# Kernel tuning notes

Measured on AMD Instinct MI355X. Metric: run time of the kernel, lower is better.

## Reference

```python
import jax, jax.numpy as jnp
import numpy as np

D_MODEL = 768
H = 12
D_K = D_MODEL // H
B = 2
S = 2048
NEG = -1e9


def setup_inputs() -> dict:
    key = jax.random.key(0)
    ks = jax.random.split(key, 12)
    scale = 1.0 / np.sqrt(D_MODEL)
    inp = {
        "q": jax.random.normal(ks[0], (B, S, D_MODEL), jnp.float32),
        "k": jax.random.normal(ks[1], (B, S, D_MODEL), jnp.float32),
        "v": jax.random.normal(ks[2], (B, S, D_MODEL), jnp.float32),
        "mask": jax.random.randint(ks[3], (B, 1, S, S), 0, 2, jnp.int32),
        "Wq": jax.random.normal(ks[4], (D_MODEL, D_MODEL), jnp.float32) * scale,
        "bq": jnp.zeros((D_MODEL,), jnp.float32),
        "Wk": jax.random.normal(ks[5], (D_MODEL, D_MODEL), jnp.float32) * scale,
        "bk": jnp.zeros((D_MODEL,), jnp.float32),
        "Wv": jax.random.normal(ks[6], (D_MODEL, D_MODEL), jnp.float32) * scale,
        "bv": jnp.zeros((D_MODEL,), jnp.float32),
        "Wo": jax.random.normal(ks[7], (D_MODEL, D_MODEL), jnp.float32) * scale,
        "bo": jnp.zeros((D_MODEL,), jnp.float32),
    }
    return inp


def _split_heads(x):
    # [B, S, D] -> [B, H, S, D_K]
    b, s, _ = x.shape
    return x.reshape(b, s, H, D_K).transpose(0, 2, 1, 3)


def reference(q, k, v, mask, Wq, bq, Wk, bk, Wv, bv, Wo, bo):
    # torch Linear: x @ W.T + b
    query = _split_heads(q @ Wq.T + bq)
    key_ = _split_heads(k @ Wk.T + bk)
    value = _split_heads(v @ Wv.T + bv)

    scores = jnp.einsum("bhqd,bhkd->bhqk", query, key_) / np.sqrt(D_K)
    scores = jnp.where(mask == 0, NEG, scores)
    attn = jax.nn.softmax(scores, axis=-1)  # dropout p=0.0 -> identity

    x = jnp.einsum("bhqk,bhkd->bhqd", attn, value)
    x = x.transpose(0, 2, 1, 3).reshape(q.shape[0], -1, D_MODEL)
    return x @ Wo.T + bo
```

## Files before the change

### kernel.cpp

```cpp
#include <hip/hip_runtime.h>
#include <math.h>

#define DMODEL 768
#define NHEAD 12
#define DKDIM 64
#define BB 2
#define SS 2048
#define MROWS (BB * SS)
#define WELEM (DMODEL * DMODEL)

typedef unsigned short bf16_t;
typedef __attribute__((ext_vector_type(8))) short s8;
typedef __attribute__((ext_vector_type(4))) float f4;

#define MFMA(a, b, c) __builtin_amdgcn_mfma_f32_16x16x32_bf16((a), (b), (c), 0, 0, 0)

__device__ __forceinline__ bf16_t f2bf(float f) {
    unsigned u = __float_as_uint(f);
    u += 0x7fffu + ((u >> 16) & 1u);
    return (bf16_t)(u >> 16);
}
__device__ __forceinline__ unsigned pack2(float a, float b) {
    return (unsigned)f2bf(a) | ((unsigned)f2bf(b) << 16);
}
__device__ __forceinline__ s8 ldfrag(const bf16_t* p) {
    union { uint4 u; s8 s; } x;
    x.u = *(const uint4*)p;
    return x.s;
}

__device__ __forceinline__ void ld_stage(const bf16_t* p, uint4& u0, uint4& u1) {
    u0 = *(const uint4*)p;
    u1 = *(const uint4*)(p + 8);
}
__device__ __forceinline__ void ld_stage(const float* p, uint4& u0, uint4& u1) {
    const float4 f0 = *(const float4*)p;
    const float4 f1 = *(const float4*)(p + 4);
    const float4 f2 = *(const float4*)(p + 8);
    const float4 f3 = *(const float4*)(p + 12);
    u0.x = pack2(f0.x, f0.y); u0.y = pack2(f0.z, f0.w);
    u0.z = pack2(f1.x, f1.y); u0.w = pack2(f1.z, f1.w);
    u1.x = pack2(f2.x, f2.y); u1.y = pack2(f2.z, f2.w);
    u1.z = pack2(f3.x, f3.y); u1.w = pack2(f3.z, f3.w);
}

__global__ void cvt_weights(const float* __restrict__ W0, const float* __restrict__ W1,
                            const float* __restrict__ W2, const float* __restrict__ W3,
                            bf16_t* __restrict__ dst)
{
    const float* src = (blockIdx.y == 0) ? W0 : (blockIdx.y == 1) ? W1
                     : (blockIdx.y == 2) ? W2 : W3;
    bf16_t* d = dst + (size_t)blockIdx.y * WELEM;
    const int i = (blockIdx.x * 256 + threadIdx.x) * 4;
    const float4 v = *(const float4*)(src + i);
    ushort4 h;
    h.x = f2bf(v.x); h.y = f2bf(v.y); h.z = f2bf(v.z); h.w = f2bf(v.w);
    *(ushort4*)(d + i) = h;
}

template<typename TA, typename TO>
__global__ __launch_bounds__(256) void gemm_tiled(
    const TA* __restrict__ A0, const TA* __restrict__ A1, const TA* __restrict__ A2,
    const bf16_t* __restrict__ W0, const bf16_t* __restrict__ W1, const bf16_t* __restrict__ W2,
    const float* __restrict__ bias0, const float* __restrict__ bias1, const float* __restrict__ bias2,
    TO* __restrict__ C0, TO* __restrict__ C1, TO* __restrict__ C2)
{
    __shared__ uint4 As4[128 * 4];
    __shared__ uint4 Bs4[128 * 4];

    const int z = blockIdx.z;
    const TA*     A    = (z == 0) ? A0 : (z == 1) ? A1 : A2;
    const bf16_t* W    = (z == 0) ? W0 : (z == 1) ? W1 : W2;
    const float*  bias = (z == 0) ? bias0 : (z == 1) ? bias1 : bias2;
    TO*           C    = (z == 0) ? C0 : (z == 1) ? C1 : C2;

    const int tid  = threadIdx.x;
    const int lane = tid & 63;
    const int w    = tid >> 6;
    const int wm   = w & 1;
    const int wn   = w >> 1;
    const int l15  = lane & 15;
    const int quad = lane >> 4;
    const int m0   = blockIdx.y * 128;
    const int n0   = blockIdx.x * 128;

    const int srow  = tid >> 1;
    const int shalf = tid & 1;
    const int sw    = srow & 3;

    const TA*     aptr = A + (size_t)(m0 + srow) * DMODEL + shalf * 16;
    const bf16_t* wptr = W + (size_t)(n0 + srow) * DMODEL + shalf * 16;

    f4 acc[4][4];
    #pragma unroll
    for (int i = 0; i < 4; i++)
        #pragma unroll
        for (int j = 0; j < 4; j++)
            acc[i][j] = (f4){0.f, 0.f, 0.f, 0.f};

    for (int k0 = 0; k0 < DMODEL; k0 += 32) {
        uint4 au0, au1, bu0, bu1;
        ld_stage(aptr + k0, au0, au1);
        ld_stage(wptr + k0, bu0, bu1);
        __syncthreads();
        As4[srow * 4 + ((shalf * 2 + 0) ^ sw)] = au0;
        As4[srow * 4 + ((shalf * 2 + 1) ^ sw)] = au1;
        Bs4[srow * 4 + ((shalf * 2 + 0) ^ sw)] = bu0;
        Bs4[srow * 4 + ((shalf * 2 + 1) ^ sw)] = bu1;
        __syncthreads();

        s8 af[4], bf[4];
        #pragma unroll
        for (int t = 0; t < 4; t++) {
            const int ar = wm * 64 + t * 16 + l15;
            const int br = wn * 64 + t * 16 + l15;
            union { uint4 u; s8 s; } xa, xb;
            xa.u = As4[ar * 4 + (quad ^ (ar & 3))];
            xb.u = Bs4[br * 4 + (quad ^ (br & 3))];
            af[t] = xa.s;
            bf[t] = xb.s;
        }
        #pragma unroll
        for (int mt = 0; mt < 4; mt++)
            #pragma unroll
            for (int nt = 0; nt < 4; nt++)
                acc[mt][nt] = MFMA(af[mt], bf[nt], acc[mt][nt]);
    }

    #pragma unroll
    for (int mt = 0; mt < 4; mt++) {
        #pragma unroll
        for (int nt = 0; nt < 4; nt++) {
            const int col = n0 + wn * 64 + nt * 16 + l15;
            const float bb = bias[col];
            #pragma unroll
            for (int reg = 0; reg < 4; reg++) {
                const int row = m0 + wm * 64 + mt * 16 + quad * 4 + reg;
                const float val = acc[mt][nt][reg] + bb;
                TO* dst = C + (size_t)row * DMODEL + col;
                if constexpr (sizeof(TO) == 2) *dst = f2bf(val);
                else                           *dst = val;
            }
        }
    }
}

__global__ __launch_bounds__(256) void attn_mfma(
    const bf16_t* __restrict__ Q, const bf16_t* __restrict__ K,
    const bf16_t* __restrict__ V, const int* __restrict__ mask,
    bf16_t* __restrict__ O)
{
    __shared__ unsigned Vs[64][36];
    __shared__ unsigned Ps[4][16][36];

    const int tid  = threadIdx.x;
    const int lane = tid & 63;
    const int w    = tid >> 6;
    const int l15  = lane & 15;
    const int quad = lane >> 4;
    const int q0   = blockIdx.x * 64;
    const int h    = blockIdx.y;
    const int b    = blockIdx.z;
    const size_t base = ((size_t)b * SS) * DMODEL + (size_t)h * DKDIM;

    const bf16_t* qrow = Q + base + (size_t)(q0 + w * 16 + l15) * DMODEL + quad * 8;
    const s8 qf0 = ldfrag(qrow);
    const s8 qf1 = ldfrag(qrow + 32);

    f4 oacc[4];
    float m_run[4], l_run[4];
    #pragma unroll
    for (int i = 0; i < 4; i++) {
        oacc[i] = (f4){0.f, 0.f, 0.f, 0.f};
        m_run[i] = -3.0e30f; l_run[i] = 0.0f;
    }

    const int kp  = tid & 31;
    const int oct = tid >> 5;

    const int* mrow = mask + (size_t)b * SS * SS + (size_t)(q0 + w * 16 + quad * 4) * SS;

    for (int k0 = 0; k0 < SS; k0 += 64) {
        const bf16_t* vrow = V + base + (size_t)(k0 + 2 * kp) * DMODEL + oct * 8;
        const uint4 va = *(const uint4*)vrow;
        const uint4 vb = *(const uint4*)(vrow + DMODEL);
        __syncthreads();
        {
            const unsigned short* pa = (const unsigned short*)&va;
            const unsigned short* pb = (const unsigned short*)&vb;
            #pragma unroll
            for (int i = 0; i < 8; i++)
                Vs[oct * 8 + i][kp] = (unsigned)pa[i] | ((unsigned)pb[i] << 16);
        }

        f4 sacc[4];
        #pragma unroll
        for (int nt = 0; nt < 4; nt++) {
            const bf16_t* krow = K + base + (size_t)(k0 + nt * 16 + l15) * DMODEL + quad * 8;
            f4 zz = {0.f, 0.f, 0.f, 0.f};
            zz = MFMA(qf0, ldfrag(krow), zz);
            zz = MFMA(qf1, ldfrag(krow + 32), zz);
            sacc[nt] = zz;
        }

        float p[4][4];
        #pragma unroll
        for (int reg = 0; reg < 4; reg++) {
            float sv[4];
            #pragma unroll
            for (int nt = 0; nt < 4; nt++) {
                const int mk = mrow[(size_t)reg * SS + k0 + nt * 16 + l15];
                sv[nt] = mk ? sacc[nt][reg] * 0.125f : -1.0e9f;
            }
            float mx = fmaxf(fmaxf(sv[0], sv[1]), fmaxf(sv[2], sv[3]));
            mx = fmaxf(mx, __shfl_xor(mx, 1, 16));
            mx = fmaxf(mx, __shfl_xor(mx, 2, 16));
            mx = fmaxf(mx, __shfl_xor(mx, 4, 16));
            mx = fmaxf(mx, __shfl_xor(mx, 8, 16));

            const float m_new = fmaxf(m_run[reg], mx);
            const float alpha = __expf(m_run[reg] - m_new);
            float rs = 0.f;
            #pragma unroll
            for (int nt = 0; nt < 4; nt++) {
                p[reg][nt] = __expf(sv[nt] - m_new);
                rs += p[reg][nt];
            }
            rs += __shfl_xor(rs, 1, 16);
            rs += __shfl_xor(rs, 2, 16);
            rs += __shfl_xor(rs, 4, 16);
            rs += __shfl_xor(rs, 8, 16);

            l_run[reg] = l_run[reg] * alpha + rs;
            m_run[reg] = m_new;
            #pragma unroll
            for (int dt = 0; dt < 4; dt++) oacc[dt][reg] *= alpha;
        }

        #pragma unroll
        for (int reg = 0; reg < 4; reg++) {
            #pragma unroll
            for (int nt = 0; nt < 4; nt++) {
                const float mine  = p[reg][nt];
                const float other = __shfl_xor(mine, 1, 16);
                if ((lane & 1) == 0)
                    Ps[w][quad * 4 + reg][nt * 8 + (l15 >> 1)] = pack2(mine, other);
            }
        }
        __syncthreads();

        #pragma unroll
        for (int kt = 0; kt < 2; kt++) {
            union { uint4 u; s8 s; } pf;
            pf.u = *(const uint4*)&Ps[w][l15][kt * 16 + quad * 4];
            #pragma unroll
            for (int dt = 0; dt < 4; dt++) {
                union { uint4 u; s8 s; } vf;
                vf.u = *(const uint4*)&Vs[dt * 16 + l15][kt * 16 + quad * 4];
                oacc[dt] = MFMA(pf.s, vf.s, oacc[dt]);
            }
        }
    }

    #pragma unroll
    for (int reg = 0; reg < 4; reg++) {
        const float inv = 1.0f / l_run[reg];
        #pragma unroll
        for (int dt = 0; dt < 4; dt++) {
            O[base + (size_t)(q0 + w * 16 + quad * 4 + reg) * DMODEL + dt * 16 + l15] =
                f2bf(oacc[dt][reg] * inv);
        }
    }
}

extern "C" void kernel_launch(void* const* d_in, const int* in_sizes, int n_in,
                              void* d_out, int out_size, void* d_ws, size_t ws_size,
                              hipStream_t stream)
{
    const float* q    = (const float*)d_in[0];
    const float* k    = (const float*)d_in[1];
    const float* v    = (const float*)d_in[2];
    const int*   mask = (const int*)  d_in[3];
    const float* Wq   = (const float*)d_in[4];
    const float* bq   = (const float*)d_in[5];
    const float* Wk   = (const float*)d_in[6];
    const float* bk   = (const float*)d_in[7];
    const float* Wv   = (const float*)d_in[8];
    const float* bv   = (const float*)d_in[9];
    const float* Wo   = (const float*)d_in[10];
    const float* bo   = (const float*)d_in[11];
    float* out = (float*)d_out;

    bf16_t* wsb = (bf16_t*)d_ws;
    const size_t plane = (size_t)MROWS * DMODEL;
    bf16_t* Qp  = wsb;
    bf16_t* Kp  = wsb + plane;
    bf16_t* Vp  = wsb + 2 * plane;
    bf16_t* Ctx = wsb + 3 * plane;
    bf16_t* Wqb = wsb + 4 * plane;
    bf16_t* Wkb = Wqb + WELEM;
    bf16_t* Wvb = Wkb + WELEM;
    bf16_t* Wob = Wvb + WELEM;

    cvt_weights<<<dim3(WELEM / 1024, 4), 256, 0, stream>>>(Wq, Wk, Wv, Wo, Wqb);

    gemm_tiled<float, bf16_t><<<dim3(DMODEL / 128, MROWS / 128, 3), 256, 0, stream>>>(
        q, k, v, Wqb, Wkb, Wvb, bq, bk, bv, Qp, Kp, Vp);

    attn_mfma<<<dim3(SS / 64, NHEAD, BB), 256, 0, stream>>>(Qp, Kp, Vp, mask, Ctx);

    gemm_tiled<bf16_t, float><<<dim3(DMODEL / 128, MROWS / 128, 1), 256, 0, stream>>>(
        Ctx, Ctx, Ctx, Wob, Wob, Wob, bo, bo, bo, out, out, out);
}
```

Baseline: 340.1 us.

## Prefetch next K/V/mask tile into registers and use per-wave V staging

The attention loop now loads the next iteration's K fragments, V rows and mask values into registers while the current tile is being processed, so global-load latency can hide behind softmax and MFMA work. Each wave keeps its own transposed copy of the V tile in shared memory, which removes both block-wide __syncthreads barriers. The launch bound now asks for 3 blocks per CU. The cost is 4x the V shared memory, redundant V loads per wave, and higher register pressure, which could lower occupancy or cause spills.

```diff
diff --git a/kernel.cpp b/kernel.cpp
--- a/kernel.cpp
+++ b/kernel.cpp
@@ -145,12 +145,12 @@
     }
 }
 
-__global__ __launch_bounds__(256) void attn_mfma(
+__global__ __launch_bounds__(256, 3) void attn_mfma(
     const bf16_t* __restrict__ Q, const bf16_t* __restrict__ K,
     const bf16_t* __restrict__ V, const int* __restrict__ mask,
     bf16_t* __restrict__ O)
 {
-    __shared__ unsigned Vs[64][36];
+    __shared__ unsigned Vs[4][64][36];
     __shared__ unsigned Ps[4][16][36];
 
     const int tid  = threadIdx.x;
@@ -175,31 +175,55 @@
         m_run[i] = -3.0e30f; l_run[i] = 0.0f;
     }
 
-    const int kp  = tid & 31;
-    const int oct = tid >> 5;
+    const int kp   = lane & 31;
+    const int half = lane >> 5;
 
     const int* mrow = mask + (size_t)b * SS * SS + (size_t)(q0 + w * 16 + quad * 4) * SS;
 
+    s8   kf[4][2];
+    uint4 vreg[4][2];
+    int  mk[4][4];
+
+    auto prefetch = [&](int kc) {
+        #pragma unroll
+        for (int nt = 0; nt < 4; nt++) {
+            const bf16_t* krow = K + base + (size_t)(kc + nt * 16 + l15) * DMODEL + quad * 8;
+            kf[nt][0] = ldfrag(krow);
+            kf[nt][1] = ldfrag(krow + 32);
+        }
+        #pragma unroll
+        for (int c = 0; c < 4; c++) {
+            const int oct = half * 4 + c;
+            const bf16_t* vrow = V + base + (size_t)(kc + 2 * kp) * DMODEL + oct * 8;
+            vreg[c][0] = *(const uint4*)vrow;
+            vreg[c][1] = *(const uint4*)(vrow + DMODEL);
+        }
+        #pragma unroll
+        for (int reg = 0; reg < 4; reg++)
+            #pragma unroll
+            for (int nt = 0; nt < 4; nt++)
+                mk[reg][nt] = mrow[(size_t)reg * SS + kc + nt * 16 + l15];
+    };
+
+    prefetch(0);
+
     for (int k0 = 0; k0 < SS; k0 += 64) {
-        const bf16_t* vrow = V + base + (size_t)(k0 + 2 * kp) * DMODEL + oct * 8;
-        const uint4 va = *(const uint4*)vrow;
-        const uint4 vb = *(const uint4*)(vrow + DMODEL);
-        __syncthreads();
-        {
-            const unsigned short* pa = (const unsigned short*)&va;
-            const unsigned short* pb = (const unsigned short*)&vb;
+        #pragma unroll
+        for (int c = 0; c < 4; c++) {
+            const int oct = half * 4 + c;
+            const unsigned short* pa = (const unsigned short*)&vreg[c][0];
+            const unsigned short* pb = (const unsigned short*)&vreg[c][1];
             #pragma unroll
             for (int i = 0; i < 8; i++)
-                Vs[oct * 8 + i][kp] = (unsigned)pa[i] | ((unsigned)pb[i] << 16);
+                Vs[w][oct * 8 + i][kp] = (unsigned)pa[i] | ((unsigned)pb[i] << 16);
         }
 
         f4 sacc[4];
         #pragma unroll
         for (int nt = 0; nt < 4; nt++) {
-            const bf16_t* krow = K + base + (size_t)(k0 + nt * 16 + l15) * DMODEL + quad * 8;
             f4 zz = {0.f, 0.f, 0.f, 0.f};
-            zz = MFMA(qf0, ldfrag(krow), zz);
-            zz = MFMA(qf1, ldfrag(krow + 32), zz);
+            zz = MFMA(qf0, kf[nt][0], zz);
+            zz = MFMA(qf1, kf[nt][1], zz);
             sacc[nt] = zz;
         }
 
@@ -208,10 +232,9 @@
         for (int reg = 0; reg < 4; reg++) {
             float sv[4];
             #pragma unroll
-            for (int nt = 0; nt < 4; nt++) {
-                const int mk = mrow[(size_t)reg * SS + k0 + nt * 16 + l15];
-                sv[nt] = mk ? sacc[nt][reg] * 0.125f : -1.0e9f;
-            }
+            for (int nt = 0; nt < 4; nt++)
+                sv[nt] = mk[reg][nt] ? sacc[nt][reg] * 0.125f : -1.0e9f;
+
             float mx = fmaxf(fmaxf(sv[0], sv[1]), fmaxf(sv[2], sv[3]));
             mx = fmaxf(mx, __shfl_xor(mx, 1, 16));
             mx = fmaxf(mx, __shfl_xor(mx, 2, 16));
@@ -237,6 +260,8 @@
             for (int dt = 0; dt < 4; dt++) oacc[dt][reg] *= alpha;
         }
 
+        prefetch((k0 + 64) & (SS - 1));
+
         #pragma unroll
         for (int reg = 0; reg < 4; reg++) {
             #pragma unroll
@@ -247,7 +272,6 @@
                     Ps[w][quad * 4 + reg][nt * 8 + (l15 >> 1)] = pack2(mine, other);
             }
         }
-        __syncthreads();
 
         #pragma unroll
         for (int kt = 0; kt < 2; kt++) {
@@ -256,7 +280,7 @@
             #pragma unroll
             for (int dt = 0; dt < 4; dt++) {
                 union { uint4 u; s8 s; } vf;
-                vf.u = *(const uint4*)&Vs[dt * 16 + l15][kt * 16 + quad * 4];
+                vf.u = *(const uint4*)&Vs[w][dt * 16 + l15][kt * 16 + quad * 4];
                 oacc[dt] = MFMA(pf.s, vf.s, oacc[dt]);
             }
         }
```

Measured after the change: 401.8 us. +18.1%, slower.

## Split attention key range across two warp groups and store V transposed

Applied to the files above, without the earlier changes.

The V projection GEMM now writes V in a per-head transposed layout, so the attention kernel can load V fragments straight from global memory without staging them in shared memory. Each attention block grows to 512 threads. Two groups of four waves each process half the key sequence for the same 64 queries, and their partial softmax states are merged through shared memory at the end. This removes the per-tile __syncthreads and V shared-memory transpose, and doubles the waves per block. In exchange it adds scattered 2-byte transposed writes in the GEMM epilogue, uncached global V loads inside the inner loop, and a larger shared-memory footprint.

```diff
diff --git a/kernel.cpp b/kernel.cpp
--- a/kernel.cpp
+++ b/kernel.cpp
@@ -8,6 +8,7 @@
 #define SS 2048
 #define MROWS (BB * SS)
 #define WELEM (DMODEL * DMODEL)
+#define CLEN 1024
 
 typedef unsigned short bf16_t;
 typedef __attribute__((ext_vector_type(8))) short s8;
@@ -137,25 +138,35 @@
             for (int reg = 0; reg < 4; reg++) {
                 const int row = m0 + wm * 64 + mt * 16 + quad * 4 + reg;
                 const float val = acc[mt][nt][reg] + bb;
-                TO* dst = C + (size_t)row * DMODEL + col;
-                if constexpr (sizeof(TO) == 2) *dst = f2bf(val);
-                else                           *dst = val;
-            }
-        }
-    }
-}
-
-__global__ __launch_bounds__(256) void attn_mfma(
+                if constexpr (sizeof(TO) == 2) {
+                    if (z == 2) {
+                        C[((((size_t)(row >> 11) * NHEAD + (col >> 6)) * DKDIM
+                            + (col & 63)) << 11) + (row & 2047)] = f2bf(val);
+                    } else {
+                        C[(size_t)row * DMODEL + col] = f2bf(val);
+                    }
+                } else {
+                    C[(size_t)row * DMODEL + col] = val;
+                }
+            }
+        }
+    }
+}
+
+__global__ __launch_bounds__(512, 6) void attn_split(
     const bf16_t* __restrict__ Q, const bf16_t* __restrict__ K,
-    const bf16_t* __restrict__ V, const int* __restrict__ mask,
-    bf16_t* __restrict__ O)
+    const bf16_t* __restrict__ Vt, const int* __restrict__ mask,
+    bf16_t* __restrict__ Ctx)
 {
-    __shared__ unsigned Vs[64][36];
-    __shared__ unsigned Ps[4][16][36];
+    __shared__ unsigned Ps[8][16][36];
+    __shared__ float    Op[8][16][64];
+    __shared__ float    Ml[8][16][2];
 
     const int tid  = threadIdx.x;
     const int lane = tid & 63;
     const int w    = tid >> 6;
+    const int wq   = w & 3;
+    const int kbeg = (w >> 2) * CLEN;
     const int l15  = lane & 15;
     const int quad = lane >> 4;
     const int q0   = blockIdx.x * 64;
@@ -163,9 +174,11 @@
     const int b    = blockIdx.z;
     const size_t base = ((size_t)b * SS) * DMODEL + (size_t)h * DKDIM;
 
-    const bf16_t* qrow = Q + base + (size_t)(q0 + w * 16 + l15) * DMODEL + quad * 8;
+    const bf16_t* qrow = Q + base + (size_t)(q0 + wq * 16 + l15) * DMODEL + quad * 8;
     const s8 qf0 = ldfrag(qrow);
     const s8 qf1 = ldfrag(qrow + 32);
+
+    const bf16_t* vt = Vt + (((size_t)b * NHEAD + h) * DKDIM << 11);
 
     f4 oacc[4];
     float m_run[4], l_run[4];
@@ -175,24 +188,9 @@
         m_run[i] = -3.0e30f; l_run[i] = 0.0f;
     }
 
-    const int kp  = tid & 31;
-    const int oct = tid >> 5;
-
-    const int* mrow = mask + (size_t)b * SS * SS + (size_t)(q0 + w * 16 + quad * 4) * SS;
-
-    for (int k0 = 0; k0 < SS; k0 += 64) {
-        const bf16_t* vrow = V + base + (size_t)(k0 + 2 * kp) * DMODEL + oct * 8;
-        const uint4 va = *(const uint4*)vrow;
-        const uint4 vb = *(const uint4*)(vrow + DMODEL);
-        __syncthreads();
-        {
-            const unsigned short* pa = (const unsigned short*)&va;
-            const unsigned short* pb = (const unsigned short*)&vb;
-            #pragma unroll
-            for (int i = 0; i < 8; i++)
-                Vs[oct * 8 + i][kp] = (unsigned)pa[i] | ((unsigned)pb[i] << 16);
-        }
-
+    const int* mrow = mask + (size_t)b * SS * SS + (size_t)(q0 + wq * 16 + quad * 4) * SS;
+
+    for (int k0 = kbeg; k0 < kbeg + CLEN; k0 += 64) {
         f4 sacc[4];
         #pragma unroll
         for (int nt = 0; nt < 4; nt++) {
@@ -247,7 +245,6 @@
                     Ps[w][quad * 4 + reg][nt * 8 + (l15 >> 1)] = pack2(mine, other);
             }
         }
-        __syncthreads();
 
         #pragma unroll
         for (int kt = 0; kt < 2; kt++) {
@@ -255,21 +252,46 @@
             pf.u = *(const uint4*)&Ps[w][l15][kt * 16 + quad * 4];
             #pragma unroll
             for (int dt = 0; dt < 4; dt++) {
-                union { uint4 u; s8 s; } vf;
-                vf.u = *(const uint4*)&Vs[dt * 16 + l15][kt * 16 + quad * 4];
-                oacc[dt] = MFMA(pf.s, vf.s, oacc[dt]);
+                const s8 vf = ldfrag(vt + (((size_t)(dt * 16 + l15)) << 11)
+                                        + k0 + kt * 32 + quad * 8);
+                oacc[dt] = MFMA(pf.s, vf, oacc[dt]);
             }
         }
     }
 
     #pragma unroll
     for (int reg = 0; reg < 4; reg++) {
-        const float inv = 1.0f / l_run[reg];
-        #pragma unroll
-        for (int dt = 0; dt < 4; dt++) {
-            O[base + (size_t)(q0 + w * 16 + quad * 4 + reg) * DMODEL + dt * 16 + l15] =
-                f2bf(oacc[dt][reg] * inv);
-        }
+        const int r16 = quad * 4 + reg;
+        if (l15 == 0) {
+            Ml[w][r16][0] = m_run[reg];
+            Ml[w][r16][1] = l_run[reg];
+        }
+        #pragma unroll
+        for (int dt = 0; dt < 4; dt++)
+            Op[w][r16][dt * 16 + l15] = oacc[dt][reg];
+    }
+    __syncthreads();
+
+    {
+        const int row  = tid >> 3;
+        const int colg = (tid & 7) * 8;
+        const int rw   = row >> 4;
+        const int r16  = row & 15;
+
+        const float ma = Ml[rw][r16][0],     la = Ml[rw][r16][1];
+        const float mb = Ml[rw + 4][r16][0], lb = Ml[rw + 4][r16][1];
+        const float M  = fmaxf(ma, mb);
+        const float wa = __expf(ma - M);
+        const float wb = __expf(mb - M);
+        const float inv = 1.0f / (wa * la + wb * lb);
+
+        union { bf16_t h[8]; uint4 u; } out;
+        #pragma unroll
+        for (int i = 0; i < 8; i++)
+            out.h[i] = f2bf((wa * Op[rw][r16][colg + i]
+                           + wb * Op[rw + 4][r16][colg + i]) * inv);
+
+        *(uint4*)(Ctx + ((size_t)b * SS + q0 + row) * DMODEL + h * DKDIM + colg) = out.u;
     }
 }
 
@@ -295,8 +317,8 @@
     const size_t plane = (size_t)MROWS * DMODEL;
     bf16_t* Qp  = wsb;
     bf16_t* Kp  = wsb + plane;
-    bf16_t* Vp  = wsb + 2 * plane;
-    bf16_t* Ctx = wsb + 3 * plane;
+    bf16_t* Ctx = wsb + 2 * plane;
+    bf16_t* Vt  = wsb + 3 * plane;
     bf16_t* Wqb = wsb + 4 * plane;
     bf16_t* Wkb = Wqb + WELEM;
     bf16_t* Wvb = Wkb + WELEM;
@@ -305,9 +327,9 @@
     cvt_weights<<<dim3(WELEM / 1024, 4), 256, 0, stream>>>(Wq, Wk, Wv, Wo, Wqb);
 
     gemm_tiled<float, bf16_t><<<dim3(DMODEL / 128, MROWS / 128, 3), 256, 0, stream>>>(
-        q, k, v, Wqb, Wkb, Wvb, bq, bk, bv, Qp, Kp, Vp);
-
-    attn_mfma<<<dim3(SS / 64, NHEAD, BB), 256, 0, stream>>>(Qp, Kp, Vp, mask, Ctx);
+        q, k, v, Wqb, Wkb, Wvb, bq, bk, bv, Qp, Kp, Vt);
+
+    attn_split<<<dim3(SS / 64, NHEAD, BB), 512, 0, stream>>>(Qp, Kp, Vt, mask, Ctx);
 
     gemm_tiled<bf16_t, float><<<dim3(DMODEL / 128, MROWS / 128, 1), 256, 0, stream>>>(
         Ctx, Ctx, Ctx, Wob, Wob, Wob, bo, bo, bo, out, out, out);
```

Result: slower. 444.1 us (+30.6%).

## Bit-pack attention mask and split KV range across two warp groups

Applied to the files above, without the earlier changes.

Adds a kernel that packs the int32 mask into one bit per element, so the attention kernel reads 32x less mask data per (b,h) instead of rereading the full int mask for each of 12 heads. The attention kernel now uses 512 threads, with two groups of four waves each covering half the key range (split-K style). The two partial softmax states are merged through shared memory at the end. This doubles the waves per block and adds an extra pack pass and a shared-memory merge.

```diff
diff --git a/kernel.cpp b/kernel.cpp
--- a/kernel.cpp
+++ b/kernel.cpp
@@ -8,6 +8,7 @@
 #define SS 2048
 #define MROWS (BB * SS)
 #define WELEM (DMODEL * DMODEL)
+#define CLEN 1024
 
 typedef unsigned short bf16_t;
 typedef __attribute__((ext_vector_type(8))) short s8;
@@ -56,6 +57,21 @@
     ushort4 h;
     h.x = f2bf(v.x); h.y = f2bf(v.y); h.z = f2bf(v.z); h.w = f2bf(v.w);
     *(ushort4*)(d + i) = h;
+}
+
+__global__ void pack_mask(const int* __restrict__ m, unsigned* __restrict__ mb)
+{
+    const size_t o = ((size_t)blockIdx.x * 256 + threadIdx.x) * 32;
+    unsigned bits = 0;
+    #pragma unroll
+    for (int i = 0; i < 8; i++) {
+        const int4 v = *(const int4*)(m + o + i * 4);
+        bits |= (v.x ? 1u : 0u) << (i * 4 + 0);
+        bits |= (v.y ? 1u : 0u) << (i * 4 + 1);
+        bits |= (v.z ? 1u : 0u) << (i * 4 + 2);
+        bits |= (v.w ? 1u : 0u) << (i * 4 + 3);
+    }
+    mb[o >> 5] = bits;
 }
 
 template<typename TA, typename TO>
@@ -145,17 +161,26 @@
     }
 }
 
-__global__ __launch_bounds__(256) void attn_mfma(
+__global__ __launch_bounds__(512, 6) void attn_split(
     const bf16_t* __restrict__ Q, const bf16_t* __restrict__ K,
-    const bf16_t* __restrict__ V, const int* __restrict__ mask,
-    bf16_t* __restrict__ O)
-{
-    __shared__ unsigned Vs[64][36];
-    __shared__ unsigned Ps[4][16][36];
+    const bf16_t* __restrict__ V, const unsigned* __restrict__ mbits,
+    bf16_t* __restrict__ Ctx)
+{
+    __shared__ __align__(16) unsigned char smem[36864];
+    typedef unsigned vs_t[64][36];
+    typedef unsigned ps_t[16][36];
+    vs_t* Vs = (vs_t*)smem;
+    ps_t* Ps = (ps_t*)(smem + 18432);
+    typedef float op_t[16][64];
+    op_t*  Op = (op_t*)smem;
+    float* Ml = (float*)(smem + 32768);
 
     const int tid  = threadIdx.x;
     const int lane = tid & 63;
     const int w    = tid >> 6;
+    const int wq   = w & 3;
+    const int g    = w >> 2;
+    const int kbeg = g * CLEN;
     const int l15  = lane & 15;
     const int quad = lane >> 4;
     const int q0   = blockIdx.x * 64;
@@ -163,7 +188,7 @@
     const int b    = blockIdx.z;
     const size_t base = ((size_t)b * SS) * DMODEL + (size_t)h * DKDIM;
 
-    const bf16_t* qrow = Q + base + (size_t)(q0 + w * 16 + l15) * DMODEL + quad * 8;
+    const bf16_t* qrow = Q + base + (size_t)(q0 + wq * 16 + l15) * DMODEL + quad * 8;
     const s8 qf0 = ldfrag(qrow);
     const s8 qf1 = ldfrag(qrow + 32);
 
@@ -175,13 +200,15 @@
         m_run[i] = -3.0e30f; l_run[i] = 0.0f;
     }
 
-    const int kp  = tid & 31;
-    const int oct = tid >> 5;
-
-    const int* mrow = mask + (size_t)b * SS * SS + (size_t)(q0 + w * 16 + quad * 4) * SS;
-
-    for (int k0 = 0; k0 < SS; k0 += 64) {
-        const bf16_t* vrow = V + base + (size_t)(k0 + 2 * kp) * DMODEL + oct * 8;
+    const int st  = tid & 255;
+    const int sg  = tid >> 8;
+    const int kp  = st & 31;
+    const int oct = st >> 5;
+
+    const unsigned* mrow = mbits + (((size_t)b * SS + q0 + wq * 16 + quad * 4) << 6);
+
+    for (int k0 = 0; k0 < CLEN; k0 += 64) {
+        const bf16_t* vrow = V + base + (size_t)(sg * CLEN + k0 + 2 * kp) * DMODEL + oct * 8;
         const uint4 va = *(const uint4*)vrow;
         const uint4 vb = *(const uint4*)(vrow + DMODEL);
         __syncthreads();
@@ -190,13 +217,15 @@
             const unsigned short* pb = (const unsigned short*)&vb;
             #pragma unroll
             for (int i = 0; i < 8; i++)
-                Vs[oct * 8 + i][kp] = (unsigned)pa[i] | ((unsigned)pb[i] << 16);
-        }
+                Vs[sg][oct * 8 + i][kp] = (unsigned)pa[i] | ((unsigned)pb[i] << 16);
+        }
+
+        const int kk = kbeg + k0;
 
         f4 sacc[4];
         #pragma unroll
         for (int nt = 0; nt < 4; nt++) {
-            const bf16_t* krow = K + base + (size_t)(k0 + nt * 16 + l15) * DMODEL + quad * 8;
+            const bf16_t* krow = K + base + (size_t)(kk + nt * 16 + l15) * DMODEL + quad * 8;
             f4 zz = {0.f, 0.f, 0.f, 0.f};
             zz = MFMA(qf0, ldfrag(krow), zz);
             zz = MFMA(qf1, ldfrag(krow + 32), zz);
@@ -206,11 +235,13 @@
         float p[4][4];
         #pragma unroll
         for (int reg = 0; reg < 4; reg++) {
+            const uint2 bw = *(const uint2*)(mrow + (reg << 6) + (kk >> 5));
             float sv[4];
             #pragma unroll
             for (int nt = 0; nt < 4; nt++) {
-                const int mk = mrow[(size_t)reg * SS + k0 + nt * 16 + l15];
-                sv[nt] = mk ? sacc[nt][reg] * 0.125f : -1.0e9f;
+                const unsigned word = (nt & 2) ? bw.y : bw.x;
+                const unsigned keep = (word >> ((nt & 1) * 16 + l15)) & 1u;
+                sv[nt] = keep ? sacc[nt][reg] * 0.125f : -1.0e9f;
             }
             float mx = fmaxf(fmaxf(sv[0], sv[1]), fmaxf(sv[2], sv[3]));
             mx = fmaxf(mx, __shfl_xor(mx, 1, 16));
@@ -256,20 +287,49 @@
             #pragma unroll
             for (int dt = 0; dt < 4; dt++) {
                 union { uint4 u; s8 s; } vf;
-                vf.u = *(const uint4*)&Vs[dt * 16 + l15][kt * 16 + quad * 4];
+                vf.u = *(const uint4*)&Vs[g][dt * 16 + l15][kt * 16 + quad * 4];
                 oacc[dt] = MFMA(pf.s, vf.s, oacc[dt]);
             }
         }
     }
 
+    __syncthreads();
+
     #pragma unroll
     for (int reg = 0; reg < 4; reg++) {
-        const float inv = 1.0f / l_run[reg];
-        #pragma unroll
-        for (int dt = 0; dt < 4; dt++) {
-            O[base + (size_t)(q0 + w * 16 + quad * 4 + reg) * DMODEL + dt * 16 + l15] =
-                f2bf(oacc[dt][reg] * inv);
-        }
+        const int r16 = quad * 4 + reg;
+        if (l15 == 0) {
+            Ml[w * 32 + r16 * 2 + 0] = m_run[reg];
+            Ml[w * 32 + r16 * 2 + 1] = l_run[reg];
+        }
+        #pragma unroll
+        for (int dt = 0; dt < 4; dt++)
+            Op[w][r16][dt * 16 + l15] = oacc[dt][reg];
+    }
+    __syncthreads();
+
+    {
+        const int row  = tid >> 3;
+        const int colg = (tid & 7) * 8;
+        const int rw   = row >> 4;
+        const int r16  = row & 15;
+
+        const float ma = Ml[rw * 32 + r16 * 2 + 0];
+        const float la = Ml[rw * 32 + r16 * 2 + 1];
+        const float mb = Ml[(rw + 4) * 32 + r16 * 2 + 0];
+        const float lb = Ml[(rw + 4) * 32 + r16 * 2 + 1];
+        const float M  = fmaxf(ma, mb);
+        const float wa = __expf(ma - M);
+        const float wb = __expf(mb - M);
+        const float inv = 1.0f / (wa * la + wb * lb);
+
+        union { bf16_t hh[8]; uint4 u; } outv;
+        #pragma unroll
+        for (int i = 0; i < 8; i++)
+            outv.hh[i] = f2bf((wa * Op[rw][r16][colg + i]
+                             + wb * Op[rw + 4][r16][colg + i]) * inv);
+
+        *(uint4*)(Ctx + ((size_t)b * SS + q0 + row) * DMODEL + h * DKDIM + colg) = outv.u;
     }
 }
 
@@ -301,13 +361,15 @@
     bf16_t* Wkb = Wqb + WELEM;
     bf16_t* Wvb = Wkb + WELEM;
     bf16_t* Wob = Wvb + WELEM;
+    unsigned* mb = (unsigned*)(Wob + WELEM);
 
     cvt_weights<<<dim3(WELEM / 1024, 4), 256, 0, stream>>>(Wq, Wk, Wv, Wo, Wqb);
+    pack_mask<<<1024, 256, 0, stream>>>(mask, mb);
 
     gemm_tiled<float, bf16_t><<<dim3(DMODEL / 128, MROWS / 128, 3), 256, 0, stream>>>(
         q, k, v, Wqb, Wkb, Wvb, bq, bk, bv, Qp, Kp, Vp);
 
-    attn_mfma<<<dim3(SS / 64, NHEAD, BB), 256, 0, stream>>>(Qp, Kp, Vp, mask, Ctx);
+    attn_split<<<dim3(SS / 64, NHEAD, BB), 512, 0, stream>>>(Qp, Kp, Vp, mb, Ctx);
 
     gemm_tiled<bf16_t, float><<<dim3(DMODEL / 128, MROWS / 128, 1), 256, 0, stream>>>(
         Ctx, Ctx, Ctx, Wob, Wob, Wob, bo, bo, bo, out, out, out);
```

Result: slower. 365.9 us (+7.6%).
